# Performance work log

Measured on AMD Instinct MI355X. Metric: run time of the kernel, lower is better.

## Reference

```python
import jax, jax.numpy as jnp
import numpy as np

N_IN, N_OUT, KNN, N_EL = 100000, 25000, 9, 200000
B, C_IN, C_OUT = 4, 8, 16


def setup_inputs() -> dict:
    key = jax.random.key(0)
    ks = jax.random.split(key, 16)
    M = N_OUT * KNN
    inp = {
        "features": jax.random.normal(ks[0], (B, C_IN, N_IN), jnp.float32),
        "domain_points": jax.random.uniform(ks[1], (N_IN, 2), jnp.float32),
        "range_points": jax.random.uniform(ks[2], (N_OUT, 2), jnp.float32),
        # kNN structure: each range point i has exactly KNN support edges
        "eval_idx_dst": jnp.repeat(jnp.arange(N_OUT, dtype=jnp.int32), KNN),
        "eval_idx_src": jax.random.randint(ks[3], (M,), 0, N_IN, jnp.int32),
        "element_list": jax.random.randint(ks[4], (N_EL, 3), 0, N_IN, jnp.int32),
        # Siren filter MLP: 2 -> 16 x5 -> C_IN*C_OUT (outermost linear)
        "siren_w_in": jax.random.normal(ks[5], (2, 16), jnp.float32) / jnp.sqrt(2.0),
        "siren_b_in": jax.random.normal(ks[6], (16,), jnp.float32) * 0.1,
        "siren_wh": jax.random.normal(ks[7], (4, 16, 16), jnp.float32) / 4.0,
        "siren_bh": jax.random.normal(ks[8], (4, 16), jnp.float32) * 0.1,
        "siren_w_out": jax.random.normal(ks[9], (16, C_IN * C_OUT), jnp.float32) / 4.0,
        "siren_b_out": jax.random.normal(ks[10], (C_IN * C_OUT,), jnp.float32) * 0.1,
        # weight_map: 6 -> 8 -> 8 -> 8 -> 3, all sigmoid
        "wm_w0": jax.random.normal(ks[11], (6, 8), jnp.float32) / jnp.sqrt(6.0),
        "wm_b0": jnp.zeros((8,), jnp.float32),
        "wm_w1": jax.random.normal(ks[12], (8, 8), jnp.float32) / jnp.sqrt(8.0),
        "wm_b1": jnp.zeros((8,), jnp.float32),
        "wm_w2": jax.random.normal(ks[13], (8, 8), jnp.float32) / jnp.sqrt(8.0),
        "wm_b2": jnp.zeros((8,), jnp.float32),
        "wm_w3": jax.random.normal(ks[14], (8, 3), jnp.float32) / jnp.sqrt(8.0),
        "wm_b3": jnp.zeros((3,), jnp.float32),
    }
    return inp


def reference(features, domain_points, range_points, eval_idx_src, eval_idx_dst,
              element_list, siren_w_in, siren_b_in, siren_wh, siren_bh,
              siren_w_out, siren_b_out, wm_w0, wm_b0, wm_w1, wm_b1,
              wm_w2, wm_b2, wm_w3, wm_b3):
    omega_0 = 1.0
    n_in = domain_points.shape[0]
    n_out = range_points.shape[0]
    c_in = features.shape[1]
    c_out = siren_w_out.shape[1] // c_in

    # --- eval_weight_map: per-element MLP + scatter_add to per-node weights ---
    el_pts = domain_points[element_list].reshape(element_list.shape[0], -1)  # [E, 6]
    h = jax.nn.sigmoid(el_pts @ wm_w0 + wm_b0)
    h = jax.nn.sigmoid(h @ wm_w1 + wm_b1)
    h = jax.nn.sigmoid(h @ wm_w2 + wm_b2)
    el_w = jax.nn.sigmoid(h @ wm_w3 + wm_b3)  # [E, 3]
    node_w = jax.ops.segment_sum(el_w.reshape(-1), element_list.reshape(-1),
                                 num_segments=n_in)  # [N_in]
    w = node_w[eval_idx_src]  # [M]

    # --- per-edge Siren filter on relative locations ---
    locs = range_points[eval_idx_dst] - domain_points[eval_idx_src]  # [M, 2]
    h = jnp.sin(omega_0 * (locs @ siren_w_in + siren_b_in))
    for i in range(siren_wh.shape[0]):  # fixed small layer count
        h = jnp.sin(omega_0 * (h @ siren_wh[i] + siren_bh[i]))
    filt = ((h @ siren_w_out + siren_b_out)
            .reshape(-1, c_in, c_out)) / c_in  # [M, C_in, C_out]

    # --- weighted gather -> contract -> scatter (quadrature integral) ---
    gathered = features[:, :, eval_idx_src]  # [B, C_in, M]
    values = jnp.einsum('n,nij,bin->bjn', w, filt, gathered)  # [B, C_out, M]
    seg = jax.ops.segment_sum(values.transpose(2, 0, 1), eval_idx_dst,
                              num_segments=n_out)  # [N_out, B, C_out]
    return seg.transpose(1, 2, 0)  # [B, C_out, N_out]
```

## Files before the change

kernel.cpp:

```cpp
#include <hip/hip_runtime.h>

#define N_IN   100000
#define N_OUT  25000
#define KNN    9
#define N_EL   200000
#define BB     4
#define C_IN   8
#define C_OUT  16
#define M_EDGE (N_OUT * KNN)

#define DPB  28
#define EPB  (DPB * KNN)
#define SOP  65

__global__ void __launch_bounds__(256) elem_kernel(
    const int*   __restrict__ el,
    const float* __restrict__ dp,
    const float* __restrict__ w0, const float* __restrict__ b0,
    const float* __restrict__ w1, const float* __restrict__ b1,
    const float* __restrict__ w2, const float* __restrict__ b2,
    const float* __restrict__ w3, const float* __restrict__ b3,
    float* __restrict__ node_w)
{
    __shared__ float lw0[48], lb0[8], lw1[64], lb1[8], lw2[64], lb2[8],
                     lw3[24], lb3[3];
    const int tid = threadIdx.x;
    if (tid < 48) lw0[tid] = w0[tid];
    if (tid < 8)  lb0[tid] = b0[tid];
    if (tid < 64) lw1[tid] = w1[tid];
    if (tid < 8)  lb1[tid] = b1[tid];
    if (tid < 64) lw2[tid] = w2[tid];
    if (tid < 8)  lb2[tid] = b2[tid];
    if (tid < 24) lw3[tid] = w3[tid];
    if (tid < 3)  lb3[tid] = b3[tid];
    __syncthreads();

    int e = blockIdx.x * 256 + tid;
    if (e >= N_EL) return;
    int i0 = el[e*3+0], i1 = el[e*3+1], i2 = el[e*3+2];
    float2 p0 = ((const float2*)dp)[i0];
    float2 p1 = ((const float2*)dp)[i1];
    float2 p2 = ((const float2*)dp)[i2];
    float p[6] = { p0.x, p0.y, p1.x, p1.y, p2.x, p2.y };

    float h[8], h2[8];
#pragma unroll
    for (int k = 0; k < 8; ++k) {
        float t = lb0[k];
#pragma unroll
        for (int j = 0; j < 6; ++j) t = fmaf(p[j], lw0[j*8+k], t);
        h[k] = 1.f / (1.f + __expf(-t));
    }
#pragma unroll
    for (int k = 0; k < 8; ++k) {
        float t = lb1[k];
#pragma unroll
        for (int j = 0; j < 8; ++j) t = fmaf(h[j], lw1[j*8+k], t);
        h2[k] = 1.f / (1.f + __expf(-t));
    }
#pragma unroll
    for (int k = 0; k < 8; ++k) {
        float t = lb2[k];
#pragma unroll
        for (int j = 0; j < 8; ++j) t = fmaf(h2[j], lw2[j*8+k], t);
        h[k] = 1.f / (1.f + __expf(-t));
    }
    float o[3];
#pragma unroll
    for (int k = 0; k < 3; ++k) {
        float t = lb3[k];
#pragma unroll
        for (int j = 0; j < 8; ++j) t = fmaf(h[j], lw3[j*3+k], t);
        o[k] = 1.f / (1.f + __expf(-t));
    }
    atomicAdd(&node_w[i0], o[0]);
    atomicAdd(&node_w[i1], o[1]);
    atomicAdd(&node_w[i2], o[2]);
}

__global__ void __launch_bounds__(256) prep_kernel(
    const float* __restrict__ f, float* __restrict__ ft,
    const float* __restrict__ w_out, float* __restrict__ w_out_t,
    const float* __restrict__ wh, float* __restrict__ wh_t,
    float* __restrict__ node_w)
{
    int n = blockIdx.x * 256 + threadIdx.x;
    if (n < C_IN * C_OUT * 16)
        w_out_t[n] = w_out[(n & 15) * 128 + (n >> 4)];
    if (n < 4 * 256)
        wh_t[n] = wh[(n & ~255) | ((n & 15) * 16) | ((n >> 4) & 15)];
    if (n >= N_IN) return;
    node_w[n] = 0.f;
    float v[32];
#pragma unroll
    for (int c = 0; c < 32; ++c) v[c] = f[c * N_IN + n];
    float4* dst = (float4*)(ft + (size_t)n * 32);
#pragma unroll
    for (int q = 0; q < 8; ++q)
        dst[q] = make_float4(v[q], v[8+q], v[16+q], v[24+q]);
}

template <int FT>
__global__ void __launch_bounds__(256, 4) edge_kernel(
    const float* __restrict__ feat,
    const float* __restrict__ dp,
    const float* __restrict__ rp,
    const int*   __restrict__ src_idx,
    const float* __restrict__ node_w,
    const float* __restrict__ w_in,
    const float* __restrict__ b_in,
    const float* __restrict__ wh,
    const float* __restrict__ wh_t,
    const float* __restrict__ bh,
    const float* __restrict__ w_out,
    const float* __restrict__ w_out_t,
    const float* __restrict__ b_out,
    float* __restrict__ out)
{
    __shared__ float s_out[DPB * SOP];
    __shared__ float lw_out[2048];
    __shared__ float lwh[1024];
    __shared__ float lb_out[128], lbh[64], lw_in[32], lb_in[16];
    const int tid = threadIdx.x;

    if (FT) {
        float4* s4 = (float4*)lw_out;
        const float4* g4 = (const float4*)w_out_t;
        s4[tid*2]   = g4[tid*2];
        s4[tid*2+1] = g4[tid*2+1];
        ((float4*)lwh)[tid & 255] = ((const float4*)wh_t)[tid & 255];
    } else {
        for (int i = tid; i < 2048; i += 256) lw_out[i] = w_out[(i & 15) * 128 + (i >> 4)];
        for (int i = tid; i < 1024; i += 256)
            lwh[i] = wh[(i & ~255) | ((i & 15) * 16) | ((i >> 4) & 15)];
    }
    if (tid < 32) ((float4*)lb_out)[tid] = ((const float4*)b_out)[tid];
    if (tid < 16) ((float4*)lbh)[tid]   = ((const float4*)bh)[tid];
    if (tid < 8)  ((float4*)lw_in)[tid] = ((const float4*)w_in)[tid];
    if (tid < 4)  ((float4*)lb_in)[tid] = ((const float4*)b_in)[tid];
    for (int i = tid; i < DPB * SOP; i += 256) s_out[i] = 0.f;
    __syncthreads();

    const int  e     = blockIdx.x * EPB + tid;
    int        ldst  = tid / KNN;
    const int  dst   = blockIdx.x * DPB + ldst;
    const bool valid = (tid < EPB) && (dst < N_OUT);
    if (!valid) ldst = 0;
    const int  ce    = valid ? e : 0;
    const int  cdst  = valid ? dst : 0;
    const int  src   = src_idx[ce];

    const float wn    = node_w[src];
    const float scale = valid ? wn * 0.125f : 0.f;

    const float2 rpt = ((const float2*)rp)[cdst];
    const float2 dpt = ((const float2*)dp)[src];
    const float lx = rpt.x - dpt.x;
    const float ly = rpt.y - dpt.y;

    float h[16];
#pragma unroll
    for (int k = 0; k < 16; ++k)
        h[k] = __sinf(fmaf(lx, lw_in[k], fmaf(ly, lw_in[16+k], lb_in[k])));

#pragma unroll
    for (int L = 0; L < 4; ++L) {
        float h2[16];
#pragma unroll
        for (int k = 0; k < 16; ++k) {
            float t = lbh[L*16 + k];
#pragma unroll
            for (int jq = 0; jq < 4; ++jq) {
                float4 w = *(const float4*)&lwh[L*256 + k*16 + jq*4];
                t = fmaf(h[jq*4+0], w.x, t);
                t = fmaf(h[jq*4+1], w.y, t);
                t = fmaf(h[jq*4+2], w.z, t);
                t = fmaf(h[jq*4+3], w.w, t);
            }
            h2[k] = t;
        }
#pragma unroll
        for (int k = 0; k < 16; ++k) h[k] = __sinf(h2[k]);
    }

    const float4* fp4 = (const float4*)(feat + (size_t)src * 32);
#pragma unroll 1
    for (int jq = 0; jq < 4; ++jq) {
        float acc[16];
#pragma unroll
        for (int t = 0; t < 16; ++t) acc[t] = 0.f;
#pragma unroll
        for (int i = 0; i < C_IN; ++i) {
            float4 gb;
            if (FT) {
                gb = fp4[i];
            } else {
                gb = make_float4(feat[(0*8+i) * N_IN + src],
                                 feat[(1*8+i) * N_IN + src],
                                 feat[(2*8+i) * N_IN + src],
                                 feat[(3*8+i) * N_IN + src]);
            }
#pragma unroll
            for (int jj = 0; jj < 4; ++jj) {
                const int col = i*16 + jq*4 + jj;
                float4 w0 = *(const float4*)&lw_out[col*16 + 0];
                float4 w1 = *(const float4*)&lw_out[col*16 + 4];
                float4 w2 = *(const float4*)&lw_out[col*16 + 8];
                float4 w3 = *(const float4*)&lw_out[col*16 + 12];
                float f = lb_out[col];
                f = fmaf(h[0],  w0.x, f); f = fmaf(h[1],  w0.y, f);
                f = fmaf(h[2],  w0.z, f); f = fmaf(h[3],  w0.w, f);
                f = fmaf(h[4],  w1.x, f); f = fmaf(h[5],  w1.y, f);
                f = fmaf(h[6],  w1.z, f); f = fmaf(h[7],  w1.w, f);
                f = fmaf(h[8],  w2.x, f); f = fmaf(h[9],  w2.y, f);
                f = fmaf(h[10], w2.z, f); f = fmaf(h[11], w2.w, f);
                f = fmaf(h[12], w3.x, f); f = fmaf(h[13], w3.y, f);
                f = fmaf(h[14], w3.z, f); f = fmaf(h[15], w3.w, f);
                f *= scale;
                acc[0*4+jj] = fmaf(f, gb.x, acc[0*4+jj]);
                acc[1*4+jj] = fmaf(f, gb.y, acc[1*4+jj]);
                acc[2*4+jj] = fmaf(f, gb.z, acc[2*4+jj]);
                acc[3*4+jj] = fmaf(f, gb.w, acc[3*4+jj]);
            }
        }
#pragma unroll
        for (int b = 0; b < BB; ++b)
#pragma unroll
            for (int jj = 0; jj < 4; ++jj)
                atomicAdd(&s_out[ldst * SOP + b*16 + jq*4 + jj], acc[b*4+jj]);
    }
    __syncthreads();

    const int dst0 = blockIdx.x * DPB;
    for (int i = tid; i < DPB * 64; i += 256) {
        const int d = i % DPB;
        const int c = i / DPB;
        const int gdst = dst0 + d;
        if (gdst < N_OUT)
            out[(size_t)c * N_OUT + gdst] = s_out[d * SOP + c];
    }
}

extern "C" void kernel_launch(void* const* d_in, const int* in_sizes, int n_in,
                              void* d_out, int out_size, void* d_ws, size_t ws_size,
                              hipStream_t stream)
{
    (void)in_sizes; (void)n_in; (void)out_size;
    const float* features = (const float*)d_in[0];
    const float* dp       = (const float*)d_in[1];
    const float* rp       = (const float*)d_in[2];
    const int*   src_idx  = (const int*)d_in[4];
    const int*   el       = (const int*)d_in[5];
    const float* w_in     = (const float*)d_in[6];
    const float* b_in     = (const float*)d_in[7];
    const float* wh       = (const float*)d_in[8];
    const float* bh       = (const float*)d_in[9];
    const float* w_out    = (const float*)d_in[10];
    const float* b_out    = (const float*)d_in[11];
    const float* wm_w0    = (const float*)d_in[12];
    const float* wm_b0    = (const float*)d_in[13];
    const float* wm_w1    = (const float*)d_in[14];
    const float* wm_b1    = (const float*)d_in[15];
    const float* wm_w2    = (const float*)d_in[16];
    const float* wm_b2    = (const float*)d_in[17];
    const float* wm_w3    = (const float*)d_in[18];
    const float* wm_b3    = (const float*)d_in[19];
    float* out = (float*)d_out;

    size_t off0 = 0;
    size_t off1 = (off0 + (size_t)N_IN * sizeof(float) + 511) & ~(size_t)511;
    size_t off2 = (off1 + (size_t)N_IN * 32 * sizeof(float) + 511) & ~(size_t)511;
    size_t off3 = (off2 + (size_t)2048 * sizeof(float) + 511) & ~(size_t)511;
    size_t need = off3 + (size_t)1024 * sizeof(float);
    float* node_w  = (float*)((char*)d_ws + off0);
    float* feat_t  = (float*)((char*)d_ws + off1);
    float* w_out_t = (float*)((char*)d_ws + off2);
    float* wh_t    = (float*)((char*)d_ws + off3);
    const bool use_t = (ws_size >= need);

    if (use_t) {
        prep_kernel<<<(N_IN + 255) / 256, 256, 0, stream>>>(
            features, feat_t, w_out, w_out_t, wh, wh_t, node_w);
        elem_kernel<<<(N_EL + 255) / 256, 256, 0, stream>>>(
            el, dp, wm_w0, wm_b0, wm_w1, wm_b1, wm_w2, wm_b2, wm_w3, wm_b3, node_w);
        edge_kernel<1><<<(N_OUT + DPB - 1) / DPB, 256, 0, stream>>>(
            feat_t, dp, rp, src_idx, node_w,
            w_in, b_in, wh, wh_t, bh, w_out, w_out_t, b_out, out);
    } else {
        hipMemsetAsync(node_w, 0, (size_t)N_IN * sizeof(float), stream);
        elem_kernel<<<(N_EL + 255) / 256, 256, 0, stream>>>(
            el, dp, wm_w0, wm_b0, wm_w1, wm_b1, wm_w2, wm_b2, wm_w3, wm_b3, node_w);
        edge_kernel<0><<<(N_OUT + DPB - 1) / DPB, 256, 0, stream>>>(
            features, dp, rp, src_idx, node_w,
            w_in, b_in, wh, (const float*)nullptr, bh, w_out,
            (const float*)nullptr, b_out, out);
    }
}
```

Before: 289.2 us.

## Privatize node-weight atomics per XCD and add reduction kernel

```diff
diff --git a/kernel.cpp b/kernel.cpp
--- a/kernel.cpp
+++ b/kernel.cpp
@@ -7,12 +7,13 @@
 #define BB     4
 #define C_IN   8
 #define C_OUT  16
-#define M_EDGE (N_OUT * KNN)
+#define NXCD   8
 
 #define DPB  28
 #define EPB  (DPB * KNN)
 #define SOP  65
 
+template <int PART>
 __global__ void __launch_bounds__(256) elem_kernel(
     const int*   __restrict__ el,
     const float* __restrict__ dp,
@@ -20,7 +21,7 @@
     const float* __restrict__ w1, const float* __restrict__ b1,
     const float* __restrict__ w2, const float* __restrict__ b2,
     const float* __restrict__ w3, const float* __restrict__ b3,
-    float* __restrict__ node_w)
+    float* __restrict__ dst)
 {
     __shared__ float lw0[48], lb0[8], lw1[64], lb1[8], lw2[64], lb2[8],
                      lw3[24], lb3[3];
@@ -73,16 +74,37 @@
         for (int j = 0; j < 8; ++j) t = fmaf(h[j], lw3[j*3+k], t);
         o[k] = 1.f / (1.f + __expf(-t));
     }
-    atomicAdd(&node_w[i0], o[0]);
-    atomicAdd(&node_w[i1], o[1]);
-    atomicAdd(&node_w[i2], o[2]);
+
+    if (PART) {
+        unsigned xcc;
+        asm volatile("s_getreg_b32 %0, hwreg(HW_REG_XCC_ID)" : "=s"(xcc));
+        float* base = dst + (size_t)xcc * N_IN;
+        __hip_atomic_fetch_add(&base[i0], o[0], __ATOMIC_RELAXED, __HIP_MEMORY_SCOPE_WORKGROUP);
+        __hip_atomic_fetch_add(&base[i1], o[1], __ATOMIC_RELAXED, __HIP_MEMORY_SCOPE_WORKGROUP);
+        __hip_atomic_fetch_add(&base[i2], o[2], __ATOMIC_RELAXED, __HIP_MEMORY_SCOPE_WORKGROUP);
+    } else {
+        atomicAdd(&dst[i0], o[0]);
+        atomicAdd(&dst[i1], o[1]);
+        atomicAdd(&dst[i2], o[2]);
+    }
+}
+
+__global__ void __launch_bounds__(256) reduce_kernel(
+    const float* __restrict__ part, float* __restrict__ node_w)
+{
+    int n = blockIdx.x * 256 + threadIdx.x;
+    if (n >= N_IN) return;
+    float s = 0.f;
+#pragma unroll
+    for (int x = 0; x < NXCD; ++x) s += part[(size_t)x * N_IN + n];
+    node_w[n] = s;
 }
 
 __global__ void __launch_bounds__(256) prep_kernel(
     const float* __restrict__ f, float* __restrict__ ft,
     const float* __restrict__ w_out, float* __restrict__ w_out_t,
     const float* __restrict__ wh, float* __restrict__ wh_t,
-    float* __restrict__ node_w)
+    float* __restrict__ part)
 {
     int n = blockIdx.x * 256 + threadIdx.x;
     if (n < C_IN * C_OUT * 16)
@@ -90,7 +112,8 @@
     if (n < 4 * 256)
         wh_t[n] = wh[(n & ~255) | ((n & 15) * 16) | ((n >> 4) & 15)];
     if (n >= N_IN) return;
-    node_w[n] = 0.f;
+#pragma unroll
+    for (int x = 0; x < NXCD; ++x) part[(size_t)x * N_IN + n] = 0.f;
     float v[32];
 #pragma unroll
     for (int c = 0; c < 32; ++c) v[c] = f[c * N_IN + n];
@@ -163,7 +186,7 @@
     for (int k = 0; k < 16; ++k)
         h[k] = __sinf(fmaf(lx, lw_in[k], fmaf(ly, lw_in[16+k], lb_in[k])));
 
-#pragma unroll
+#pragma unroll 1
     for (int L = 0; L < 4; ++L) {
         float h2[16];
 #pragma unroll
@@ -269,26 +292,29 @@
 
     size_t off0 = 0;
     size_t off1 = (off0 + (size_t)N_IN * sizeof(float) + 511) & ~(size_t)511;
-    size_t off2 = (off1 + (size_t)N_IN * 32 * sizeof(float) + 511) & ~(size_t)511;
-    size_t off3 = (off2 + (size_t)2048 * sizeof(float) + 511) & ~(size_t)511;
-    size_t need = off3 + (size_t)1024 * sizeof(float);
+    size_t off2 = (off1 + (size_t)NXCD * N_IN * sizeof(float) + 511) & ~(size_t)511;
+    size_t off3 = (off2 + (size_t)N_IN * 32 * sizeof(float) + 511) & ~(size_t)511;
+    size_t off4 = (off3 + (size_t)2048 * sizeof(float) + 511) & ~(size_t)511;
+    size_t need = off4 + (size_t)1024 * sizeof(float);
     float* node_w  = (float*)((char*)d_ws + off0);
-    float* feat_t  = (float*)((char*)d_ws + off1);
-    float* w_out_t = (float*)((char*)d_ws + off2);
-    float* wh_t    = (float*)((char*)d_ws + off3);
+    float* part    = (float*)((char*)d_ws + off1);
+    float* feat_t  = (float*)((char*)d_ws + off2);
+    float* w_out_t = (float*)((char*)d_ws + off3);
+    float* wh_t    = (float*)((char*)d_ws + off4);
     const bool use_t = (ws_size >= need);
 
     if (use_t) {
         prep_kernel<<<(N_IN + 255) / 256, 256, 0, stream>>>(
-            features, feat_t, w_out, w_out_t, wh, wh_t, node_w);
-        elem_kernel<<<(N_EL + 255) / 256, 256, 0, stream>>>(
-            el, dp, wm_w0, wm_b0, wm_w1, wm_b1, wm_w2, wm_b2, wm_w3, wm_b3, node_w);
+            features, feat_t, w_out, w_out_t, wh, wh_t, part);
+        elem_kernel<1><<<(N_EL + 255) / 256, 256, 0, stream>>>(
+            el, dp, wm_w0, wm_b0, wm_w1, wm_b1, wm_w2, wm_b2, wm_w3, wm_b3, part);
+        reduce_kernel<<<(N_IN + 255) / 256, 256, 0, stream>>>(part, node_w);
         edge_kernel<1><<<(N_OUT + DPB - 1) / DPB, 256, 0, stream>>>(
             feat_t, dp, rp, src_idx, node_w,
             w_in, b_in, wh, wh_t, bh, w_out, w_out_t, b_out, out);
     } else {
         hipMemsetAsync(node_w, 0, (size_t)N_IN * sizeof(float), stream);
-        elem_kernel<<<(N_EL + 255) / 256, 256, 0, stream>>>(
+        elem_kernel<0><<<(N_EL + 255) / 256, 256, 0, stream>>>(
             el, dp, wm_w0, wm_b0, wm_w1, wm_b1, wm_w2, wm_b2, wm_w3, wm_b3, node_w);
         edge_kernel<0><<<(N_OUT + DPB - 1) / DPB, 256, 0, stream>>>(
             features, dp, rp, src_idx, node_w,
```

Measured after the change: 288.1 us. Within noise of the previous version (-0.4%).
